# Performance work log

Hardware: AMD Instinct MI355X
Metric: run time of the kernel (lower is better)

The kernel has to match this reference:

```python
import jax, jax.numpy as jnp
import numpy as np

D = 768
NH = 8
HD = D // NH
DFF = 2048
EPS = 1e-5


def _layer_norm(x, g, b):
    mu = jnp.mean(x, axis=-1, keepdims=True)
    var = jnp.mean(jnp.square(x - mu), axis=-1, keepdims=True)
    return (x - mu) * jax.lax.rsqrt(var + EPS) * g + b


def setup_inputs() -> dict:
    key = jax.random.key(0)
    ks = jax.random.split(key, 16)
    B, L = 2, 2048
    s = 0.02
    return {
        "x": jax.random.normal(ks[0], (B, L, D), jnp.float32),
        "attn_bias": jax.random.normal(ks[1], (B, L, L), jnp.float32),
        "in_proj_w": jax.random.normal(ks[2], (3 * D, D), jnp.float32) * s,
        "in_proj_b": jnp.zeros((3 * D,), jnp.float32),
        "out_w": jax.random.normal(ks[3], (D, D), jnp.float32) * s,
        "out_b": jnp.zeros((D,), jnp.float32),
        "W1": jax.random.normal(ks[4], (DFF, D), jnp.float32) * s,
        "b1": jnp.zeros((DFF,), jnp.float32),
        "W2": jax.random.normal(ks[5], (D, DFF), jnp.float32) * s,
        "b2": jnp.zeros((D,), jnp.float32),
        "g1": jnp.ones((D,), jnp.float32),
        "be1": jnp.zeros((D,), jnp.float32),
        "g2": jnp.ones((D,), jnp.float32),
        "be2": jnp.zeros((D,), jnp.float32),
    }


def reference(x, attn_bias, in_proj_w, in_proj_b, out_w, out_b,
              W1, b1, W2, b2, g1, be1, g2, be2):
    B, L, _ = x.shape
    # fused qkv projection (torch nn.MultiheadAttention in_proj)
    qkv = x @ in_proj_w.T + in_proj_b          # [B, L, 3D]
    q, k, v = jnp.split(qkv, 3, axis=-1)
    q = q.reshape(B, L, NH, HD).transpose(0, 2, 1, 3)  # [B, nH, L, hd]
    k = k.reshape(B, L, NH, HD).transpose(0, 2, 1, 3)
    v = v.reshape(B, L, NH, HD).transpose(0, 2, 1, 3)
    scale = 1.0 / jnp.sqrt(jnp.asarray(HD, x.dtype))
    scores = jnp.einsum("bhqd,bhkd->bhqk", q * scale, k)
    scores = scores + attn_bias[:, None, :, :]         # broadcast over heads == expand
    attn = jax.nn.softmax(scores, axis=-1)
    ctx = jnp.einsum("bhqk,bhkd->bhqd", attn, v)       # [B, nH, L, hd]
    ctx = ctx.transpose(0, 2, 1, 3).reshape(B, L, D)
    attn_out = ctx @ out_w.T + out_b
    x = _layer_norm(x + attn_out, g1, be1)
    h = jax.nn.gelu(x @ W1.T + b1, approximate=False)  # torch default GELU = erf
    ff = h @ W2.T + b2
    return _layer_norm(x + ff, g2, be2)
```

## Files before the change

### kernel.cpp

```cpp
#include <hip/hip_runtime.h>
#include <hip/hip_bf16.h>
#include <math.h>

typedef __bf16 bf16;
typedef __attribute__((ext_vector_type(8))) __bf16 bf16x8;
typedef __attribute__((ext_vector_type(4))) __bf16 bf16x4;
typedef __attribute__((ext_vector_type(2))) __bf16 bf16x2;
typedef __attribute__((ext_vector_type(4))) float f32x4;

#define LOG2E 1.4426950408889634f

__device__ __forceinline__ void gload16(const bf16* g, bf16* l) {
  __builtin_amdgcn_global_load_lds(
      (const __attribute__((address_space(1))) void*)g,
      (__attribute__((address_space(3))) void*)l, 16, 0, 0);
}

__device__ __forceinline__ unsigned packbf2(float a, float b) {
  bf16x2 v = { (bf16)a, (bf16)b };
  return __builtin_bit_cast(unsigned, v);
}

struct CastSegs { const float* src[5]; bf16* dst[5]; };

__global__ void fused_cast_kernel(CastSegs segs) {
  const int e0 = 786432, e1 = 1228800, e2 = 1376256, e3 = 1769472, e4 = 2162688;
  int i = blockIdx.x * blockDim.x + threadIdx.x;
  int stride = gridDim.x * blockDim.x;
  for (; i < e4; i += stride) {
    int s = 0, base = 0;
    if (i >= e0) { s = 1; base = e0; }
    if (i >= e1) { s = 2; base = e1; }
    if (i >= e2) { s = 3; base = e2; }
    if (i >= e3) { s = 4; base = e3; }
    float4 v = ((const float4*)segs.src[s])[i - base];
    bf16x4 o = { (bf16)v.x, (bf16)v.y, (bf16)v.z, (bf16)v.w };
    ((bf16x4*)segs.dst[s])[i - base] = o;
  }
}

template<int MODE>
__launch_bounds__(256)
__global__ void gemm_kernel(const bf16* __restrict__ A, const bf16* __restrict__ W,
                            const float* __restrict__ bias, bf16* __restrict__ vt,
                            void* __restrict__ out, int K, int O) {
  __shared__ bf16 As[128 * 64];
  __shared__ bf16 Bs[128 * 64];
  const int t    = threadIdx.x;
  const int lane = t & 63;
  const int wave = t >> 6;
  const int wr = (wave >> 1) * 64;
  const int wc = (wave & 1) * 64;
  const int n0 = blockIdx.y * 128;
  const int o0 = blockIdx.x * 128;

  f32x4 zero = {0.f, 0.f, 0.f, 0.f};
  f32x4 acc[4][4];
#pragma unroll
  for (int m = 0; m < 4; m++)
#pragma unroll
    for (int n = 0; n < 4; n++) acc[m][n] = zero;

  const int fr  = lane & 15;
  const int fg8 = (lane >> 4) * 8;

  for (int k0 = 0; k0 < K; k0 += 64) {
    __syncthreads();
#pragma unroll
    for (int c = 0; c < 4; c++) {
      int f = c * 256 + t;
      int row = f >> 3;
      int col = (f & 7) * 8;
      gload16(&A[(size_t)(n0 + row) * K + k0 + col], &As[f * 8]);
      gload16(&W[(size_t)(o0 + row) * K + k0 + col], &Bs[f * 8]);
    }
    __syncthreads();
#pragma unroll
    for (int kf = 0; kf < 2; kf++) {
      bf16x8 a[4], b[4];
#pragma unroll
      for (int m = 0; m < 4; m++) a[m] = *(const bf16x8*)&As[(wr + m * 16 + fr) * 64 + kf * 32 + fg8];
#pragma unroll
      for (int n = 0; n < 4; n++) b[n] = *(const bf16x8*)&Bs[(wc + n * 16 + fr) * 64 + kf * 32 + fg8];
#pragma unroll
      for (int m = 0; m < 4; m++)
#pragma unroll
        for (int n = 0; n < 4; n++)
          acc[m][n] = __builtin_amdgcn_mfma_f32_16x16x32_bf16(a[m], b[n], acc[m][n], 0, 0, 0);
    }
  }

  const int fg4 = (lane >> 4) * 4;
#pragma unroll
  for (int m = 0; m < 4; m++) {
#pragma unroll
    for (int n = 0; n < 4; n++) {
      int col = o0 + wc + n * 16 + fr;
      float bv = bias[col];
      if constexpr (MODE == 3) {
        if (col >= 1536) {
          int c = col - 1536;
          int h = c / 96;
          int hd = c - h * 96;
          int row0 = n0 + wr + m * 16 + fg4;
          int b = row0 >> 11;
          int token = row0 & 2047;
          bf16x4 ov;
#pragma unroll
          for (int r = 0; r < 4; r++) ov[r] = (bf16)(acc[m][n][r] + bv);
          *(bf16x4*)&vt[((size_t)((b * 8 + h) * 96 + hd)) * 2048 + token] = ov;
          continue;
        }
      }
#pragma unroll
      for (int r = 0; r < 4; r++) {
        int row = n0 + wr + m * 16 + fg4 + r;
        float v = acc[m][n][r] + bv;
        if constexpr (MODE == 2) {
          v = 0.5f * v * (1.0f + erff(v * 0.70710678118654752f));
          ((bf16*)out)[(size_t)row * O + col] = (bf16)v;
        } else {
          ((bf16*)out)[(size_t)row * O + col] = (bf16)v;
        }
      }
    }
  }
}

__launch_bounds__(256)
__global__ void gemmW_kernel(const bf16* __restrict__ A, const bf16* __restrict__ W,
                             const float* __restrict__ bias, const float* __restrict__ res,
                             float* __restrict__ out, int K, int O) {
  __shared__ bf16 As[128 * 64];
  __shared__ bf16 Bs[64 * 64];
  const int t    = threadIdx.x;
  const int lane = t & 63;
  const int wave = t >> 6;
  const int wr = wave * 32;
  const int n0 = blockIdx.y * 128;
  const int o0 = blockIdx.x * 64;

  f32x4 zero = {0.f, 0.f, 0.f, 0.f};
  f32x4 acc[2][4];
#pragma unroll
  for (int m = 0; m < 2; m++)
#pragma unroll
    for (int n = 0; n < 4; n++) acc[m][n] = zero;

  const int fr  = lane & 15;
  const int fg8 = (lane >> 4) * 8;

  for (int k0 = 0; k0 < K; k0 += 64) {
    __syncthreads();
#pragma unroll
    for (int c = 0; c < 4; c++) {
      int f = c * 256 + t;
      int row = f >> 3;
      int col = (f & 7) * 8;
      gload16(&A[(size_t)(n0 + row) * K + k0 + col], &As[f * 8]);
    }
#pragma unroll
    for (int c = 0; c < 2; c++) {
      int f = c * 256 + t;
      int row = f >> 3;
      int col = (f & 7) * 8;
      gload16(&W[(size_t)(o0 + row) * K + k0 + col], &Bs[f * 8]);
    }
    __syncthreads();
#pragma unroll
    for (int kf = 0; kf < 2; kf++) {
      bf16x8 a[2], b[4];
#pragma unroll
      for (int m = 0; m < 2; m++) a[m] = *(const bf16x8*)&As[(wr + m * 16 + fr) * 64 + kf * 32 + fg8];
#pragma unroll
      for (int n = 0; n < 4; n++) b[n] = *(const bf16x8*)&Bs[(n * 16 + fr) * 64 + kf * 32 + fg8];
#pragma unroll
      for (int m = 0; m < 2; m++)
#pragma unroll
        for (int n = 0; n < 4; n++)
          acc[m][n] = __builtin_amdgcn_mfma_f32_16x16x32_bf16(a[m], b[n], acc[m][n], 0, 0, 0);
    }
  }

  const int fg4 = (lane >> 4) * 4;
#pragma unroll
  for (int m = 0; m < 2; m++) {
#pragma unroll
    for (int n = 0; n < 4; n++) {
      int col = o0 + n * 16 + fr;
      float bv = bias[col];
#pragma unroll
      for (int r = 0; r < 4; r++) {
        int row = n0 + wr + m * 16 + fg4 + r;
        float v = acc[m][n][r] + bv + res[(size_t)row * O + col];
        out[(size_t)row * O + col] = v;
      }
    }
  }
}

__launch_bounds__(256, 4)
__global__ void attn_kernel(const bf16* __restrict__ qkv, const bf16* __restrict__ vt,
                            const float* __restrict__ bias, float* __restrict__ opart,
                            float* __restrict__ ml) {
  __shared__ bf16 Ks[64 * 104];
  __shared__ bf16 Vs[96 * 104];
  const int t    = threadIdx.x;
  const int lane = t & 63;
  const int wave = t >> 6;
  const int qb = blockIdx.x, h = blockIdx.y;
  const int half = blockIdx.z & 1, b = blockIdx.z >> 1;
  const int kvstart = half * 1024;
  const int q0 = qb * 64 + wave * 16;
  const int fq = lane & 15;
  const int g  = lane >> 4;
  const size_t base = (size_t)b * 2048 * 2304;

  bf16x8 qf[3];
  {
    const bf16* qp = qkv + base + (size_t)(q0 + fq) * 2304 + h * 96;
#pragma unroll
    for (int f = 0; f < 3; f++) qf[f] = *(const bf16x8*)(qp + f * 32 + g * 8);
  }

  const int krow = t >> 2, kcb = (t & 3) * 24;
  const bf16* kbase = qkv + base + (size_t)kvstart * 2304 + 768 + h * 96;
  const bf16* vbase = vt + (size_t)((b * 8 + h) * 96) * 2048 + kvstart;

  bf16x8 kreg[3], vreg[3];
#pragma unroll
  for (int i = 0; i < 3; i++) {
    kreg[i] = *(const bf16x8*)(kbase + (size_t)krow * 2304 + kcb + i * 8);
    int c = t + 256 * i;
    vreg[i] = *(const bf16x8*)(vbase + (size_t)(c >> 3) * 2048 + (c & 7) * 8);
  }

  float m_run = -1e30f, l_run = 0.f;
  f32x4 zero = {0.f, 0.f, 0.f, 0.f};
  f32x4 o_acc[6];
#pragma unroll
  for (int i = 0; i < 6; i++) o_acc[i] = zero;

  const float scale = 0.10206207261596575f;
  const float* bp = bias + ((size_t)b * 2048 + q0 + fq) * 2048 + kvstart;

  for (int kv0 = 0; kv0 < 1024; kv0 += 64) {
    if (kv0) __syncthreads();
    *(bf16x8*)&Ks[krow * 104 + kcb]      = kreg[0];
    *(bf16x8*)&Ks[krow * 104 + kcb + 8]  = kreg[1];
    *(bf16x8*)&Ks[krow * 104 + kcb + 16] = kreg[2];
#pragma unroll
    for (int i = 0; i < 3; i++) {
      int c = t + 256 * i;
      *(bf16x8*)&Vs[(c >> 3) * 104 + (c & 7) * 8] = vreg[i];
    }
    if (kv0 + 64 < 1024) {
      int nx = kv0 + 64;
#pragma unroll
      for (int i = 0; i < 3; i++) {
        kreg[i] = *(const bf16x8*)(kbase + (size_t)(nx + krow) * 2304 + kcb + i * 8);
        int c = t + 256 * i;
        vreg[i] = *(const bf16x8*)(vbase + (size_t)(c >> 3) * 2048 + nx + (c & 7) * 8);
      }
    }
    __builtin_amdgcn_sched_barrier(0);
    __syncthreads();

    float4 bfv[4];
#pragma unroll
    for (int kvt = 0; kvt < 4; kvt++)
      bfv[kvt] = *(const float4*)(bp + kv0 + kvt * 16 + g * 4);

    f32x4 s[4];
#pragma unroll
    for (int kvt = 0; kvt < 4; kvt++) {
      s[kvt] = zero;
#pragma unroll
      for (int f = 0; f < 3; f++) {
        bf16x8 kfr = *(const bf16x8*)&Ks[(kvt * 16 + fq) * 104 + f * 32 + g * 8];
        s[kvt] = __builtin_amdgcn_mfma_f32_16x16x32_bf16(kfr, qf[f], s[kvt], 0, 0, 0);
      }
    }

    float p[4][4];
    float vmax = -1e30f;
#pragma unroll
    for (int kvt = 0; kvt < 4; kvt++)
#pragma unroll
      for (int r = 0; r < 4; r++) {
        float sv = fmaf(s[kvt][r], scale, (&bfv[kvt].x)[r]);
        p[kvt][r] = sv;
        vmax = fmaxf(vmax, sv);
      }
    vmax = fmaxf(vmax, __shfl_xor(vmax, 16));
    vmax = fmaxf(vmax, __shfl_xor(vmax, 32));
    if (!__all(vmax <= m_run + 8.0f)) {
      float m_new = fmaxf(m_run, vmax);
      float corr = exp2f((m_run - m_new) * LOG2E);
      l_run *= corr;
#pragma unroll
      for (int i = 0; i < 6; i++)
#pragma unroll
        for (int r = 0; r < 4; r++) o_acc[i][r] *= corr;
      m_run = m_new;
    }
    float rsum = 0.f;
    uint2 d[4];
#pragma unroll
    for (int kvt = 0; kvt < 4; kvt++) {
      float e0 = exp2f((p[kvt][0] - m_run) * LOG2E);
      float e1 = exp2f((p[kvt][1] - m_run) * LOG2E);
      float e2 = exp2f((p[kvt][2] - m_run) * LOG2E);
      float e3 = exp2f((p[kvt][3] - m_run) * LOG2E);
      rsum += (e0 + e1) + (e2 + e3);
      d[kvt].x = packbf2(e0, e1);
      d[kvt].y = packbf2(e2, e3);
    }
    rsum += __shfl_xor(rsum, 16);
    rsum += __shfl_xor(rsum, 32);
    l_run += rsum;

    bf16x8 pb[2];
    {
      bool glow = (g < 2);
      uint2 snd0 = glow ? d[1] : d[0];
      uint2 snd1 = glow ? d[3] : d[2];
      uint2 r0, r1;
      r0.x = __shfl_xor(snd0.x, 32); r0.y = __shfl_xor(snd0.y, 32);
      r1.x = __shfl_xor(snd1.x, 32); r1.y = __shfl_xor(snd1.y, 32);
      uint2 k0 = glow ? d[0] : d[1];
      uint2 k1 = glow ? d[2] : d[3];
      bool sendk = ((g ^ (g >> 1)) & 1);
      uint2 s0 = sendk ? k0 : r0;
      uint2 s1 = sendk ? k1 : r1;
      uint2 q0_, q1_;
      q0_.x = __shfl_xor(s0.x, 16); q0_.y = __shfl_xor(s0.y, 16);
      q1_.x = __shfl_xor(s1.x, 16); q1_.y = __shfl_xor(s1.y, 16);
      uint2 kept0 = sendk ? r0 : k0;
      uint2 kept1 = sendk ? r1 : k1;
      bool godd = (g & 1);
      uint2 lo0 = godd ? q0_ : kept0;
      uint2 hi0 = godd ? kept0 : q0_;
      uint2 lo1 = godd ? q1_ : kept1;
      uint2 hi1 = godd ? kept1 : q1_;
      uint4 u0 = { lo0.x, lo0.y, hi0.x, hi0.y };
      uint4 u1 = { lo1.x, lo1.y, hi1.x, hi1.y };
      pb[0] = __builtin_bit_cast(bf16x8, u0);
      pb[1] = __builtin_bit_cast(bf16x8, u1);
    }

#pragma unroll
    for (int kf = 0; kf < 2; kf++) {
#pragma unroll
      for (int ht = 0; ht < 6; ht++) {
        bf16x8 vfr = *(const bf16x8*)&Vs[(ht * 16 + fq) * 104 + kf * 32 + g * 8];
        o_acc[ht] = __builtin_amdgcn_mfma_f32_16x16x32_bf16(vfr, pb[kf], o_acc[ht], 0, 0, 0);
      }
    }
  }

  {
    int q = q0 + fq;
    float* op = opart + (size_t)half * (16 * 2048 * 96) + ((size_t)(b * 8 + h) * 2048 + q) * 96;
    float* mlp = ml + ((size_t)half * 32768 + (size_t)(b * 8 + h) * 2048 + q) * 2;
#pragma unroll
    for (int ht = 0; ht < 6; ht++)
      *(f32x4*)&op[ht * 16 + g * 4] = o_acc[ht];
    if (g == 0) { mlp[0] = m_run; mlp[1] = l_run; }
  }
}

__launch_bounds__(256)
__global__ void attn_combine_kernel(const float* __restrict__ opart, const float* __restrict__ ml,
                                    bf16* __restrict__ ctx) {
  int idx = blockIdx.x * blockDim.x + threadIdx.x;
  if (idx >= 786432) return;
  int e = idx * 4;
  int bh = e / (2048 * 96);
  int rem = e - bh * (2048 * 96);
  int q = rem / 96;
  int hd = rem - q * 96;
  const float* op0 = opart;
  const float* op1 = opart + (size_t)16 * 2048 * 96;
  float4 o1 = *(const float4*)&op0[e];
  float4 o2 = *(const float4*)&op1[e];
  const float* ml0 = ml + (size_t)(bh * 2048 + q) * 2;
  const float* ml1 = ml0 + (size_t)32768 * 2;
  float m1 = ml0[0], l1 = ml0[1];
  float m2 = ml1[0], l2 = ml1[1];
  float M = fmaxf(m1, m2);
  float w1 = exp2f((m1 - M) * LOG2E);
  float w2 = exp2f((m2 - M) * LOG2E);
  float inv = 1.0f / (l1 * w1 + l2 * w2);
  int b = bh >> 3, h = bh & 7;
  bf16x4 o;
  o[0] = (bf16)((o1.x * w1 + o2.x * w2) * inv);
  o[1] = (bf16)((o1.y * w1 + o2.y * w2) * inv);
  o[2] = (bf16)((o1.z * w1 + o2.z * w2) * inv);
  o[3] = (bf16)((o1.w * w1 + o2.w * w2) * inv);
  *(bf16x4*)&ctx[((size_t)b * 2048 + q) * 768 + h * 96 + hd] = o;
}

__launch_bounds__(256)
__global__ void ln_kernel(const float* in, const float* __restrict__ gamma,
                          const float* __restrict__ beta, float* outf, bf16* outb) {
  const int row = blockIdx.x;
  const int t = threadIdx.x;
  const float* rp = in + (size_t)row * 768;
  float v[3];
#pragma unroll
  for (int i = 0; i < 3; i++) v[i] = rp[t + 256 * i];
  float s = v[0] + v[1] + v[2];
  float ss = v[0] * v[0] + v[1] * v[1] + v[2] * v[2];
#pragma unroll
  for (int off = 1; off < 64; off <<= 1) {
    s += __shfl_xor(s, off);
    ss += __shfl_xor(ss, off);
  }
  __shared__ float red[8];
  if ((t & 63) == 0) { red[(t >> 6) * 2] = s; red[(t >> 6) * 2 + 1] = ss; }
  __syncthreads();
  s = red[0] + red[2] + red[4] + red[6];
  ss = red[1] + red[3] + red[5] + red[7];
  float mu = s * (1.0f / 768.0f);
  float var = ss * (1.0f / 768.0f) - mu * mu;
  float rs = rsqrtf(var + 1e-5f);
#pragma unroll
  for (int i = 0; i < 3; i++) {
    int col = t + 256 * i;
    float y = (v[i] - mu) * rs * gamma[col] + beta[col];
    outf[(size_t)row * 768 + col] = y;
    if (outb) outb[(size_t)row * 768 + col] = (bf16)y;
  }
}

extern "C" void kernel_launch(void* const* d_in, const int* in_sizes, int n_in,
                              void* d_out, int out_size, void* d_ws, size_t ws_size,
                              hipStream_t stream) {
  (void)in_sizes; (void)n_in; (void)out_size; (void)ws_size;
  const float* x     = (const float*)d_in[0];
  const float* ab    = (const float*)d_in[1];
  const float* w_qkv = (const float*)d_in[2];
  const float* b_qkv = (const float*)d_in[3];
  const float* w_out = (const float*)d_in[4];
  const float* b_out = (const float*)d_in[5];
  const float* W1    = (const float*)d_in[6];
  const float* b1    = (const float*)d_in[7];
  const float* W2    = (const float*)d_in[8];
  const float* b2    = (const float*)d_in[9];
  const float* g1    = (const float*)d_in[10];
  const float* be1   = (const float*)d_in[11];
  const float* g2    = (const float*)d_in[12];
  const float* be2   = (const float*)d_in[13];
  float* outf = (float*)d_out;

  char* p = (char*)d_ws;
  bf16* xb    = (bf16*)p;  p += (size_t)4096 * 768 * 2;
  bf16* qkv   = (bf16*)p;  p += (size_t)4096 * 2304 * 2;
  bf16* ctx   = (bf16*)p;  p += (size_t)4096 * 768 * 2;
  float* x1f  = (float*)p; p += (size_t)4096 * 768 * 4;
  bf16* x1b   = (bf16*)p;  p += (size_t)4096 * 768 * 2;
  bf16* hbuf  = (bf16*)p;  p += (size_t)4096 * 2048 * 2;
  bf16* wqkvb = (bf16*)p;  p += (size_t)2304 * 768 * 2;
  bf16* woutb = (bf16*)p;  p += (size_t)768 * 768 * 2;
  bf16* w1b   = (bf16*)p;  p += (size_t)2048 * 768 * 2;
  bf16* w2b   = (bf16*)p;  p += (size_t)768 * 2048 * 2;
  float* opart = (float*)p; p += (size_t)2 * 16 * 2048 * 96 * 4;
  float* mlb   = (float*)p; p += (size_t)2 * 32768 * 2 * 4;
  bf16* vtb   = (bf16*)x1f;

  CastSegs segs;
  segs.src[0] = x;     segs.dst[0] = xb;
  segs.src[1] = w_qkv; segs.dst[1] = wqkvb;
  segs.src[2] = w_out; segs.dst[2] = woutb;
  segs.src[3] = W1;    segs.dst[3] = w1b;
  segs.src[4] = W2;    segs.dst[4] = w2b;
  fused_cast_kernel<<<2048, 256, 0, stream>>>(segs);

  gemm_kernel<3><<<dim3(18, 32), 256, 0, stream>>>(xb, wqkvb, b_qkv, vtb, qkv, 768, 2304);
  attn_kernel<<<dim3(32, 8, 4), 256, 0, stream>>>(qkv, vtb, ab, opart, mlb);
  attn_combine_kernel<<<3072, 256, 0, stream>>>(opart, mlb, ctx);
  gemmW_kernel<<<dim3(12, 32), 256, 0, stream>>>(ctx, woutb, b_out, x, outf, 768, 768);
  ln_kernel<<<4096, 256, 0, stream>>>(outf, g1, be1, x1f, x1b);
  gemm_kernel<2><<<dim3(16, 32), 256, 0, stream>>>(x1b, w1b, b1, nullptr, hbuf, 768, 2048);
  gemmW_kernel<<<dim3(12, 32), 256, 0, stream>>>(hbuf, w2b, b2, x1f, outf, 2048, 768);
  ln_kernel<<<4096, 256, 0, stream>>>(outf, g2, be2, outf, nullptr);
}
```

Measured before the change: 224.1 us.

## Split-K output GEMMs, fuse bias/residual into LayerNorm, add XCD swizzle and MFMA priority

The two N=768 projection GEMMs are replaced by a 128x128-tile split-K kernel with two K halves. Each half writes fp32 partials, and a new LayerNorm kernel sums the partials, bias and residual before normalising. Block IDs in the GEMM and attention kernels are remapped so neighbouring tiles land on the same XCD for L2 reuse, and s_setprio is raised around the MFMA sections in attention. The split-K path adds extra fp32 partial traffic (two 12MB buffers written and read) in exchange for larger tiles and fewer, better-filled blocks.

```diff
diff --git a/kernel.cpp b/kernel.cpp
--- a/kernel.cpp
+++ b/kernel.cpp
@@ -19,6 +19,10 @@
 __device__ __forceinline__ unsigned packbf2(float a, float b) {
   bf16x2 v = { (bf16)a, (bf16)b };
   return __builtin_bit_cast(unsigned, v);
+}
+
+__device__ __forceinline__ int xcd_swz(int id, int nwg) {
+  return (id & 7) * (nwg >> 3) + (id >> 3);
 }
 
 struct CastSegs { const float* src[5]; bf16* dst[5]; };
@@ -46,13 +50,16 @@
                             void* __restrict__ out, int K, int O) {
   __shared__ bf16 As[128 * 64];
   __shared__ bf16 Bs[128 * 64];
+  const int gx = gridDim.x;
+  const int id = blockIdx.y * gx + blockIdx.x;
+  const int swz = xcd_swz(id, gx * gridDim.y);
+  const int n0 = (swz / gx) * 128;
+  const int o0 = (swz % gx) * 128;
   const int t    = threadIdx.x;
   const int lane = t & 63;
   const int wave = t >> 6;
   const int wr = (wave >> 1) * 64;
   const int wc = (wave & 1) * 64;
-  const int n0 = blockIdx.y * 128;
-  const int o0 = blockIdx.x * 128;
 
   f32x4 zero = {0.f, 0.f, 0.f, 0.f};
   f32x4 acc[4][4];
@@ -128,29 +135,34 @@
 }
 
 __launch_bounds__(256)
-__global__ void gemmW_kernel(const bf16* __restrict__ A, const bf16* __restrict__ W,
-                             const float* __restrict__ bias, const float* __restrict__ res,
-                             float* __restrict__ out, int K, int O) {
+__global__ void gemmSK_kernel(const bf16* __restrict__ A, const bf16* __restrict__ W,
+                              float* __restrict__ out, int K, int O) {
   __shared__ bf16 As[128 * 64];
-  __shared__ bf16 Bs[64 * 64];
+  __shared__ bf16 Bs[128 * 64];
+  const int gx = gridDim.x;
+  const int id = blockIdx.y * gx + blockIdx.x;
+  const int swz = xcd_swz(id, gx * gridDim.y);
+  const int n0 = (swz / gx) * 128;
+  const int o0 = (swz % gx) * 128;
   const int t    = threadIdx.x;
   const int lane = t & 63;
   const int wave = t >> 6;
-  const int wr = wave * 32;
-  const int n0 = blockIdx.y * 128;
-  const int o0 = blockIdx.x * 64;
+  const int wr = (wave >> 1) * 64;
+  const int wc = (wave & 1) * 64;
+  const int khalf = K >> 1;
+  const int kbeg = blockIdx.z * khalf;
 
   f32x4 zero = {0.f, 0.f, 0.f, 0.f};
-  f32x4 acc[2][4];
-#pragma unroll
-  for (int m = 0; m < 2; m++)
+  f32x4 acc[4][4];
+#pragma unroll
+  for (int m = 0; m < 4; m++)
 #pragma unroll
     for (int n = 0; n < 4; n++) acc[m][n] = zero;
 
   const int fr  = lane & 15;
   const int fg8 = (lane >> 4) * 8;
 
-  for (int k0 = 0; k0 < K; k0 += 64) {
+  for (int k0 = kbeg; k0 < kbeg + khalf; k0 += 64) {
     __syncthreads();
 #pragma unroll
     for (int c = 0; c < 4; c++) {
@@ -158,42 +170,35 @@
       int row = f >> 3;
       int col = (f & 7) * 8;
       gload16(&A[(size_t)(n0 + row) * K + k0 + col], &As[f * 8]);
-    }
-#pragma unroll
-    for (int c = 0; c < 2; c++) {
-      int f = c * 256 + t;
-      int row = f >> 3;
-      int col = (f & 7) * 8;
       gload16(&W[(size_t)(o0 + row) * K + k0 + col], &Bs[f * 8]);
     }
     __syncthreads();
 #pragma unroll
     for (int kf = 0; kf < 2; kf++) {
-      bf16x8 a[2], b[4];
-#pragma unroll
-      for (int m = 0; m < 2; m++) a[m] = *(const bf16x8*)&As[(wr + m * 16 + fr) * 64 + kf * 32 + fg8];
-#pragma unroll
-      for (int n = 0; n < 4; n++) b[n] = *(const bf16x8*)&Bs[(n * 16 + fr) * 64 + kf * 32 + fg8];
-#pragma unroll
-      for (int m = 0; m < 2; m++)
+      bf16x8 a[4], b[4];
+#pragma unroll
+      for (int m = 0; m < 4; m++) a[m] = *(const bf16x8*)&As[(wr + m * 16 + fr) * 64 + kf * 32 + fg8];
+#pragma unroll
+      for (int n = 0; n < 4; n++) b[n] = *(const bf16x8*)&Bs[(wc + n * 16 + fr) * 64 + kf * 32 + fg8];
+#pragma unroll
+      for (int m = 0; m < 4; m++)
 #pragma unroll
         for (int n = 0; n < 4; n++)
           acc[m][n] = __builtin_amdgcn_mfma_f32_16x16x32_bf16(a[m], b[n], acc[m][n], 0, 0, 0);
     }
   }
 
+  float* op = out + (size_t)blockIdx.z * 4096 * O;
   const int fg4 = (lane >> 4) * 4;
 #pragma unroll
-  for (int m = 0; m < 2; m++) {
+  for (int m = 0; m < 4; m++) {
 #pragma unroll
     for (int n = 0; n < 4; n++) {
-      int col = o0 + n * 16 + fr;
-      float bv = bias[col];
+      int col = o0 + wc + n * 16 + fr;
 #pragma unroll
       for (int r = 0; r < 4; r++) {
         int row = n0 + wr + m * 16 + fg4 + r;
-        float v = acc[m][n][r] + bv + res[(size_t)row * O + col];
-        out[(size_t)row * O + col] = v;
+        op[(size_t)row * O + col] = acc[m][n][r];
       }
     }
   }
@@ -208,8 +213,13 @@
   const int t    = threadIdx.x;
   const int lane = t & 63;
   const int wave = t >> 6;
-  const int qb = blockIdx.x, h = blockIdx.y;
-  const int half = blockIdx.z & 1, b = blockIdx.z >> 1;
+  const int bid = blockIdx.x;
+  const int xcd = bid & 7, j = bid >> 3;
+  const int h = j & 7;
+  const int g_ = xcd * 16 + (j >> 3);
+  const int qb = g_ & 31;
+  const int bh = g_ >> 5;
+  const int half = bh & 1, b = bh >> 1;
   const int kvstart = half * 1024;
   const int q0 = qb * 64 + wave * 16;
   const int fq = lane & 15;
@@ -272,6 +282,7 @@
       bfv[kvt] = *(const float4*)(bp + kv0 + kvt * 16 + g * 4);
 
     f32x4 s[4];
+    __builtin_amdgcn_s_setprio(1);
 #pragma unroll
     for (int kvt = 0; kvt < 4; kvt++) {
       s[kvt] = zero;
@@ -281,6 +292,7 @@
         s[kvt] = __builtin_amdgcn_mfma_f32_16x16x32_bf16(kfr, qf[f], s[kvt], 0, 0, 0);
       }
     }
+    __builtin_amdgcn_s_setprio(0);
 
     float p[4][4];
     float vmax = -1e30f;
@@ -349,6 +361,7 @@
       pb[1] = __builtin_bit_cast(bf16x8, u1);
     }
 
+    __builtin_amdgcn_s_setprio(1);
 #pragma unroll
     for (int kf = 0; kf < 2; kf++) {
 #pragma unroll
@@ -357,6 +370,7 @@
         o_acc[ht] = __builtin_amdgcn_mfma_f32_16x16x32_bf16(vfr, pb[kf], o_acc[ht], 0, 0, 0);
       }
     }
+    __builtin_amdgcn_s_setprio(0);
   }
 
   {
@@ -402,20 +416,25 @@
 }
 
 __launch_bounds__(256)
-__global__ void ln_kernel(const float* in, const float* __restrict__ gamma,
-                          const float* __restrict__ beta, float* outf, bf16* outb) {
+__global__ void lnf_kernel(const float* __restrict__ p0, const float* __restrict__ p1,
+                           const float* __restrict__ bias, const float* __restrict__ res,
+                           const float* __restrict__ gamma, const float* __restrict__ beta,
+                           float* __restrict__ outf, bf16* __restrict__ outb) {
   const int row = blockIdx.x;
   const int t = threadIdx.x;
-  const float* rp = in + (size_t)row * 768;
+  const size_t off = (size_t)row * 768;
   float v[3];
 #pragma unroll
-  for (int i = 0; i < 3; i++) v[i] = rp[t + 256 * i];
+  for (int i = 0; i < 3; i++) {
+    int col = t + 256 * i;
+    v[i] = p0[off + col] + p1[off + col] + bias[col] + res[off + col];
+  }
   float s = v[0] + v[1] + v[2];
   float ss = v[0] * v[0] + v[1] * v[1] + v[2] * v[2];
 #pragma unroll
-  for (int off = 1; off < 64; off <<= 1) {
-    s += __shfl_xor(s, off);
-    ss += __shfl_xor(ss, off);
+  for (int o = 1; o < 64; o <<= 1) {
+    s += __shfl_xor(s, o);
+    ss += __shfl_xor(ss, o);
   }
   __shared__ float red[8];
   if ((t & 63) == 0) { red[(t >> 6) * 2] = s; red[(t >> 6) * 2 + 1] = ss; }
@@ -429,8 +448,8 @@
   for (int i = 0; i < 3; i++) {
     int col = t + 256 * i;
     float y = (v[i] - mu) * rs * gamma[col] + beta[col];
-    outf[(size_t)row * 768 + col] = y;
-    if (outb) outb[(size_t)row * 768 + col] = (bf16)y;
+    outf[off + col] = y;
+    if (outb) outb[off + col] = (bf16)y;
   }
 }
 
@@ -468,6 +487,7 @@
   float* opart = (float*)p; p += (size_t)2 * 16 * 2048 * 96 * 4;
   float* mlb   = (float*)p; p += (size_t)2 * 32768 * 2 * 4;
   bf16* vtb   = (bf16*)x1f;
+  float* pSK  = opart;
 
   CastSegs segs;
   segs.src[0] = x;     segs.dst[0] = xb;
@@ -478,11 +498,11 @@
   fused_cast_kernel<<<2048, 256, 0, stream>>>(segs);
 
   gemm_kernel<3><<<dim3(18, 32), 256, 0, stream>>>(xb, wqkvb, b_qkv, vtb, qkv, 768, 2304);
-  attn_kernel<<<dim3(32, 8, 4), 256, 0, stream>>>(qkv, vtb, ab, opart, mlb);
+  attn_kernel<<<1024, 256, 0, stream>>>(qkv, vtb, ab, opart, mlb);
   attn_combine_kernel<<<3072, 256, 0, stream>>>(opart, mlb, ctx);
-  gemmW_kernel<<<dim3(12, 32), 256, 0, stream>>>(ctx, woutb, b_out, x, outf, 768, 768);
-  ln_kernel<<<4096, 256, 0, stream>>>(outf, g1, be1, x1f, x1b);
+  gemmSK_kernel<<<dim3(6, 32, 2), 256, 0, stream>>>(ctx, woutb, pSK, 768, 768);
+  lnf_kernel<<<4096, 256, 0, stream>>>(pSK, pSK + (size_t)4096 * 768, b_out, x, g1, be1, x1f, x1b);
   gemm_kernel<2><<<dim3(16, 32), 256, 0, stream>>>(x1b, w1b, b1, nullptr, hbuf, 768, 2048);
-  gemmW_kernel<<<dim3(12, 32), 256, 0, stream>>>(hbuf, w2b, b2, x1f, outf, 2048, 768);
-  ln_kernel<<<4096, 256, 0, stream>>>(outf, g2, be2, outf, nullptr);
-}
+  gemmSK_kernel<<<dim3(6, 32, 2), 256, 0, stream>>>(hbuf, w2b, pSK, 2048, 768);
+  lnf_kernel<<<4096, 256, 0, stream>>>(pSK, pSK + (size_t)4096 * 768, b2, x1f, g2, be2, outf, nullptr);
+}
```

After: 217.0 us. 1.03x faster.
